# Optimization experiments

Hardware: AMD Instinct MI355X
Metric: run time of the kernel (lower is better)

## Reference

```python
import jax, jax.numpy as jnp
import numpy as np

B, S, D = 4, 1024, 512
H, DK, DV = 8, 64, 64
MAX_POS = 8  # relative position clamp; w_rpr maps d_k -> max_pos+1
EPS = 1e-6
TEMP = DK ** 0.5


def setup_inputs() -> dict:
    key = jax.random.key(0)
    ks = jax.random.split(key, 10)
    inp = {
        "q": jax.random.normal(ks[0], (B, S, D), jnp.float32),
        "k": jax.random.normal(ks[1], (B, S, D), jnp.float32),
        "v": jax.random.normal(ks[2], (B, S, D), jnp.float32),
        "dist": jax.random.randint(ks[3], (B, S, S), 0, 9, jnp.int32),
        # parameters (stored [in, out]; torch Linear applies x @ W.T)
        "Wq": jax.random.normal(ks[4], (D, H * DK), jnp.float32) / np.sqrt(D),
        "Wk": jax.random.normal(ks[5], (D, H * DK), jnp.float32) / np.sqrt(D),
        "Wv": jax.random.normal(ks[6], (D, H * DV), jnp.float32) / np.sqrt(D),
        "Wrpr": jax.random.normal(ks[7], (DK, MAX_POS + 1), jnp.float32) / np.sqrt(DK),
        "Wo": jax.random.normal(ks[8], (H * DV, D), jnp.float32) / np.sqrt(H * DV),
        "ln_g": jnp.ones((D,), jnp.float32),
        "ln_b": jnp.zeros((D,), jnp.float32),
    }
    return inp


def reference(q, k, v, dist, Wq, Wk, Wv, Wrpr, Wo, ln_g, ln_b):
    residual = q
    # LayerNorm on queries only (as in the original forward)
    mu = jnp.mean(q, axis=-1, keepdims=True)
    var = jnp.var(q, axis=-1, keepdims=True)
    qn = (q - mu) / jnp.sqrt(var + EPS) * ln_g + ln_b

    # projections -> [B, H, S, d]
    qh = (qn @ Wq).reshape(B, S, H, DK).transpose(0, 2, 1, 3) / TEMP
    kh = (k @ Wk).reshape(B, S, H, DK).transpose(0, 2, 1, 3)
    vh = (v @ Wv).reshape(B, S, H, DV).transpose(0, 2, 1, 3)

    # content scores [B,H,S,S]
    attn_k = jnp.einsum("bhqd,bhkd->bhqk", qh, kh)

    # relative-position bias: project q onto rpr embeddings then gather per (query, key)
    q_dot_rpr = qh @ Wrpr  # [B,H,S,max_pos+1]
    pos = jnp.minimum(dist, MAX_POS)  # [B,S,S]
    idx = jnp.broadcast_to(pos[:, None], (B, H, S, S))
    attn_rpr = jnp.take_along_axis(q_dot_rpr, idx, axis=-1)  # [B,H,S,S]

    attn = jax.nn.softmax(attn_k + attn_rpr, axis=-1)
    out = jnp.einsum("bhqk,bhkd->bhqd", attn, vh)  # [B,H,S,DV]
    out = out.transpose(0, 2, 1, 3).reshape(B, S, H * DV)
    out = out @ Wo + residual
    return out, attn
```

## Files before the change

kernel.cpp:

```cpp
#include <hip/hip_runtime.h>

#define BB 4
#define SS 1024
#define DDIM 512
#define HH 8
#define NR 9
#define QB 16
#define EPSV 1e-6f

typedef __attribute__((ext_vector_type(8))) short bf16x8;
typedef __attribute__((ext_vector_type(4))) short short4v;
typedef __attribute__((ext_vector_type(4))) float f32x4;

struct HL { short h; short l; };

__device__ inline float bfv(short h) {
    union { unsigned u; float f; } b; b.u = ((unsigned)(unsigned short)h) << 16; return b.f;
}
__device__ inline HL split2(float x) {
    union { float f; unsigned u; } a; a.f = x;
    unsigned short hu = (unsigned short)(a.u >> 16);
    union { unsigned u; float f; } b; b.u = ((unsigned)hu) << 16;
    float r = x - b.f;
    union { float f; unsigned u; } c; c.f = r;
    HL o; o.h = (short)hu; o.l = (short)(c.u >> 16);
    return o;
}

__global__ __launch_bounds__(128) void ln_split(const float* __restrict__ q,
                                                const float* __restrict__ g,
                                                const float* __restrict__ b,
                                                short* __restrict__ yh,
                                                short* __restrict__ yl) {
    int row = blockIdx.x;
    const float* x = q + (size_t)row * DDIM;
    int t = threadIdx.x;
    float4 v = ((const float4*)x)[t];
    float s  = v.x + v.y + v.z + v.w;
    float ss = v.x*v.x + v.y*v.y + v.z*v.z + v.w*v.w;
    __shared__ float rs[128], rss[128];
    rs[t] = s; rss[t] = ss; __syncthreads();
    for (int o = 64; o > 0; o >>= 1) {
        if (t < o) { rs[t] += rs[t+o]; rss[t] += rss[t+o]; }
        __syncthreads();
    }
    float mu  = rs[0] * (1.0f/DDIM);
    float var = rss[0] * (1.0f/DDIM) - mu*mu;
    float inv = rsqrtf(var + EPSV);
    float4 gg = ((const float4*)g)[t];
    float4 bb = ((const float4*)b)[t];
    float o0 = (v.x-mu)*inv*gg.x + bb.x;
    float o1 = (v.y-mu)*inv*gg.y + bb.y;
    float o2 = (v.z-mu)*inv*gg.z + bb.z;
    float o3 = (v.w-mu)*inv*gg.w + bb.w;
    short4v h4, l4;
    HL t0 = split2(o0); h4[0] = t0.h; l4[0] = t0.l;
    HL t1 = split2(o1); h4[1] = t1.h; l4[1] = t1.l;
    HL t2 = split2(o2); h4[2] = t2.h; l4[2] = t2.l;
    HL t3 = split2(o3); h4[3] = t3.h; l4[3] = t3.l;
    *(short4v*)&yh[(size_t)row*DDIM + t*4] = h4;
    *(short4v*)&yl[(size_t)row*DDIM + t*4] = l4;
}

__global__ __launch_bounds__(256) void split_x(const float* __restrict__ x,
                                               short* __restrict__ xh,
                                               short* __restrict__ xl) {
    int i = blockIdx.x*256 + threadIdx.x;
    float4 v = ((const float4*)x)[i];
    short4v h4, l4;
    HL t0 = split2(v.x); h4[0] = t0.h; l4[0] = t0.l;
    HL t1 = split2(v.y); h4[1] = t1.h; l4[1] = t1.l;
    HL t2 = split2(v.z); h4[2] = t2.h; l4[2] = t2.l;
    HL t3 = split2(v.w); h4[3] = t3.h; l4[3] = t3.l;
    *(short4v*)&xh[(size_t)i*4] = h4;
    *(short4v*)&xl[(size_t)i*4] = l4;
}

__global__ __launch_bounds__(256) void transW(const float* __restrict__ W,
                                              short* __restrict__ wth,
                                              short* __restrict__ wtl) {
    __shared__ float T[64][65];
    int n0 = blockIdx.x*64, k0 = blockIdx.y*64;
    int t = threadIdx.x;
    int kr = t >> 4, nc = (t & 15)*4;
#pragma unroll
    for (int i = 0; i < 4; ++i) {
        float4 v = *(const float4*)&W[(size_t)(k0 + kr + i*16)*DDIM + n0 + nc];
        T[nc+0][kr+i*16] = v.x;
        T[nc+1][kr+i*16] = v.y;
        T[nc+2][kr+i*16] = v.z;
        T[nc+3][kr+i*16] = v.w;
    }
    __syncthreads();
    int nr = t >> 2, kq = (t & 3)*16;
    short h8[16], l8[16];
#pragma unroll
    for (int j = 0; j < 16; ++j) {
        HL tt = split2(T[nr][kq+j]); h8[j] = tt.h; l8[j] = tt.l;
    }
    size_t base = (size_t)(n0+nr)*DDIM + k0 + kq;
#pragma unroll
    for (int j = 0; j < 2; ++j) {
        bf16x8 hv, lv;
#pragma unroll
        for (int e = 0; e < 8; ++e) { hv[e] = h8[j*8+e]; lv[e] = l8[j*8+e]; }
        *(bf16x8*)&wth[base + j*8] = hv;
        *(bf16x8*)&wtl[base + j*8] = lv;
    }
}

__global__ __launch_bounds__(256) void mm_gemm_qkv(
        const short* __restrict__ qnh, const short* __restrict__ qnl,
        const short* __restrict__ kxh, const short* __restrict__ kxl,
        const short* __restrict__ vxh, const short* __restrict__ vxl,
        const short* __restrict__ WqTh, const short* __restrict__ WqTl,
        const short* __restrict__ WkTh, const short* __restrict__ WkTl,
        const short* __restrict__ WvTh, const short* __restrict__ WvTl,
        short* __restrict__ qh_hi, short* __restrict__ qh_lo,
        short* __restrict__ kh_hi, short* __restrict__ kh_lo,
        short* __restrict__ vT_hi, short* __restrict__ vT_lo) {
    int z = blockIdx.z;
    const short *Ahi, *Alo, *Bhi, *Blo;
    short *o_hi, *o_lo;
    float scale = 1.0f;
    if (z == 0) { Ahi=qnh; Alo=qnl; Bhi=WqTh; Blo=WqTl; o_hi=qh_hi; o_lo=qh_lo; scale=0.125f; }
    else if (z == 1) { Ahi=kxh; Alo=kxl; Bhi=WkTh; Blo=WkTl; o_hi=kh_hi; o_lo=kh_lo; }
    else { Ahi=vxh; Alo=vxl; Bhi=WvTh; Blo=WvTl; o_hi=vT_hi; o_lo=vT_lo; }

    int n0 = blockIdx.x * 64, m0 = blockIdx.y * 64;
    int tid = threadIdx.x;
    int lane = tid & 63, w = tid >> 6;
    int wr = w >> 1, wc = w & 1;
    int r = lane & 15, ko = (lane >> 4) * 8;
    f32x4 acc[2][2] = {};
    int arow0 = m0 + wr*32 + r;
    int brow0 = n0 + wc*32 + r;
    for (int k0 = 0; k0 < 512; k0 += 32) {
        bf16x8 ah[2], al[2], bh[2], bl[2];
#pragma unroll
        for (int i = 0; i < 2; ++i) {
            size_t aoff = (size_t)(arow0 + i*16)*512 + k0 + ko;
            ah[i] = *(const bf16x8*)&Ahi[aoff];
            al[i] = *(const bf16x8*)&Alo[aoff];
            size_t boff = (size_t)(brow0 + i*16)*512 + k0 + ko;
            bh[i] = *(const bf16x8*)&Bhi[boff];
            bl[i] = *(const bf16x8*)&Blo[boff];
        }
#pragma unroll
        for (int i = 0; i < 2; ++i)
#pragma unroll
            for (int j = 0; j < 2; ++j) {
                acc[i][j] = __builtin_amdgcn_mfma_f32_16x16x32_bf16(ah[i], bh[j], acc[i][j], 0, 0, 0);
                acc[i][j] = __builtin_amdgcn_mfma_f32_16x16x32_bf16(ah[i], bl[j], acc[i][j], 0, 0, 0);
                acc[i][j] = __builtin_amdgcn_mfma_f32_16x16x32_bf16(al[i], bh[j], acc[i][j], 0, 0, 0);
            }
    }
    int rb = (lane >> 4) * 4;
    int cf = lane & 15;
#pragma unroll
    for (int i = 0; i < 2; ++i)
#pragma unroll
        for (int j = 0; j < 2; ++j)
#pragma unroll
            for (int rr = 0; rr < 4; ++rr) {
                int m = m0 + wr*32 + i*16 + rb + rr;
                int n = n0 + wc*32 + j*16 + cf;
                float v = acc[i][j][rr] * scale;
                HL tt = split2(v);
                int b = m >> 10, s = m & 1023;
                int hh = n >> 6, d = n & 63;
                size_t off;
                if (z == 2) off = ((size_t)((b*HH + hh)*64 + d))*SS + s;
                else        off = ((size_t)((b*HH + hh)*SS + s))*64 + d;
                o_hi[off] = tt.h;
                o_lo[off] = tt.l;
            }
}

__global__ __launch_bounds__(256) void mm_gemm_o(const short* __restrict__ Ahi,
                                                 const short* __restrict__ Alo,
                                                 const short* __restrict__ Bhi,
                                                 const short* __restrict__ Blo,
                                                 const float* __restrict__ res,
                                                 float* __restrict__ o_f) {
    int n0 = blockIdx.x * 64, m0 = blockIdx.y * 64;
    int tid = threadIdx.x;
    int lane = tid & 63, w = tid >> 6;
    int wr = w >> 1, wc = w & 1;
    int r = lane & 15, ko = (lane >> 4) * 8;
    f32x4 acc[2][2] = {};
    int arow0 = m0 + wr*32 + r;
    int brow0 = n0 + wc*32 + r;
    for (int k0 = 0; k0 < 512; k0 += 32) {
        bf16x8 ah[2], al[2], bh[2], bl[2];
#pragma unroll
        for (int i = 0; i < 2; ++i) {
            size_t aoff = (size_t)(arow0 + i*16)*512 + k0 + ko;
            ah[i] = *(const bf16x8*)&Ahi[aoff];
            al[i] = *(const bf16x8*)&Alo[aoff];
            size_t boff = (size_t)(brow0 + i*16)*512 + k0 + ko;
            bh[i] = *(const bf16x8*)&Bhi[boff];
            bl[i] = *(const bf16x8*)&Blo[boff];
        }
#pragma unroll
        for (int i = 0; i < 2; ++i)
#pragma unroll
            for (int j = 0; j < 2; ++j) {
                acc[i][j] = __builtin_amdgcn_mfma_f32_16x16x32_bf16(ah[i], bh[j], acc[i][j], 0, 0, 0);
                acc[i][j] = __builtin_amdgcn_mfma_f32_16x16x32_bf16(ah[i], bl[j], acc[i][j], 0, 0, 0);
                acc[i][j] = __builtin_amdgcn_mfma_f32_16x16x32_bf16(al[i], bh[j], acc[i][j], 0, 0, 0);
            }
    }
    int rb = (lane >> 4) * 4;
    int cf = lane & 15;
#pragma unroll
    for (int i = 0; i < 2; ++i)
#pragma unroll
        for (int j = 0; j < 2; ++j)
#pragma unroll
            for (int rr = 0; rr < 4; ++rr) {
                int m = m0 + wr*32 + i*16 + rb + rr;
                int n = n0 + wc*32 + j*16 + cf;
                o_f[(size_t)m*512 + n] = acc[i][j][rr] + res[(size_t)m*512 + n];
            }
}

__global__ __launch_bounds__(256) void qdr_kernel(const short* __restrict__ qhi,
                                                  const short* __restrict__ qlo,
                                                  const float* __restrict__ Wrpr,
                                                  float* __restrict__ qdr) {
    __shared__ float w[64*NR];
    int t = threadIdx.x;
    for (int i = t; i < 64*NR; i += 256) w[i] = Wrpr[i];
    __syncthreads();
    int row = blockIdx.x*256 + t;
    const short* qh = qhi + (size_t)row*64;
    const short* ql = qlo + (size_t)row*64;
    float acc[NR] = {};
#pragma unroll
    for (int d4 = 0; d4 < 16; ++d4) {
        short4v h4 = *(const short4v*)&qh[d4*4];
        short4v l4 = *(const short4v*)&ql[d4*4];
#pragma unroll
        for (int j = 0; j < 4; ++j) {
            float x = bfv(h4[j]) + bfv(l4[j]);
            const float* wr2 = &w[(d4*4+j)*NR];
#pragma unroll
            for (int p = 0; p < NR; ++p) acc[p] += x * wr2[p];
        }
    }
#pragma unroll
    for (int p = 0; p < NR; ++p) qdr[(size_t)row*NR + p] = acc[p];
}

__global__ __launch_bounds__(512, 4) void fused_attn(
        const short* __restrict__ qhi, const short* __restrict__ qlo,
        const short* __restrict__ khi, const short* __restrict__ klo,
        const short* __restrict__ vThi, const short* __restrict__ vTlo,
        const float* __restrict__ qdr,
        const int* __restrict__ dist,
        float* __restrict__ attn,
        short* __restrict__ pv_hi, short* __restrict__ pv_lo) {
    __shared__ float S_T[SS][QB+1];
    __shared__ float qd[QB][NR];
    __shared__ float inv_s[QB];
    __shared__ float PC[QB][68];
    int bh = blockIdx.y, b = bh >> 3, h = bh & 7;
    int q0 = blockIdx.x * QB;
    int tid = threadIdx.x, lane = tid & 63, w = tid >> 6;
    int r = lane & 15, g = lane >> 4, ko = g*8;

    if (tid < QB*NR) qd[tid/NR][tid%NR] = qdr[((size_t)bh*SS + q0)*NR + tid];

    const short* Qh = qhi + (size_t)bh*SS*64;
    const short* Ql = qlo + (size_t)bh*SS*64;
    const short* Kh = khi + (size_t)bh*SS*64;
    const short* Kl = klo + (size_t)bh*SS*64;
    {
        f32x4 acc[8];
#pragma unroll
        for (int t2 = 0; t2 < 8; ++t2) acc[t2] = (f32x4){0.f,0.f,0.f,0.f};
#pragma unroll
        for (int ks = 0; ks < 64; ks += 32) {
            bf16x8 ah = *(const bf16x8*)&Qh[(size_t)(q0+r)*64 + ks + ko];
            bf16x8 al = *(const bf16x8*)&Ql[(size_t)(q0+r)*64 + ks + ko];
#pragma unroll
            for (int ct = 0; ct < 8; ++ct) {
                int kc = w*128 + ct*16 + r;
                bf16x8 bh2 = *(const bf16x8*)&Kh[(size_t)kc*64 + ks + ko];
                bf16x8 bl2 = *(const bf16x8*)&Kl[(size_t)kc*64 + ks + ko];
                acc[ct] = __builtin_amdgcn_mfma_f32_16x16x32_bf16(ah, bh2, acc[ct], 0, 0, 0);
                acc[ct] = __builtin_amdgcn_mfma_f32_16x16x32_bf16(ah, bl2, acc[ct], 0, 0, 0);
                acc[ct] = __builtin_amdgcn_mfma_f32_16x16x32_bf16(al, bh2, acc[ct], 0, 0, 0);
            }
        }
#pragma unroll
        for (int ct = 0; ct < 8; ++ct)
#pragma unroll
            for (int rr = 0; rr < 4; ++rr)
                S_T[w*128 + ct*16 + r][g*4 + rr] = acc[ct][rr];
    }
    __syncthreads();

    int row = tid >> 5, c32 = tid & 31;
    const int* drow = &dist[((size_t)b*SS + q0 + row)*SS];
    float m = -1e30f;
    f32x4 sv[8];
#pragma unroll
    for (int c = 0; c < 8; ++c) {
        int col = c32*4 + c*128;
        int4 d4 = *(const int4*)&drow[col];
        f32x4 s4;
        s4[0] = S_T[col+0][row] + qd[row][d4.x > 8 ? 8 : d4.x];
        s4[1] = S_T[col+1][row] + qd[row][d4.y > 8 ? 8 : d4.y];
        s4[2] = S_T[col+2][row] + qd[row][d4.z > 8 ? 8 : d4.z];
        s4[3] = S_T[col+3][row] + qd[row][d4.w > 8 ? 8 : d4.w];
        sv[c] = s4;
        m = fmaxf(m, fmaxf(fmaxf(s4[0], s4[1]), fmaxf(s4[2], s4[3])));
    }
#pragma unroll
    for (int o = 1; o < 32; o <<= 1) m = fmaxf(m, __shfl_xor(m, o));
    float sum = 0.f;
#pragma unroll
    for (int c = 0; c < 8; ++c) {
        int col = c32*4 + c*128;
        f32x4 p4 = sv[c];
        p4[0] = expf(p4[0]-m); p4[1] = expf(p4[1]-m);
        p4[2] = expf(p4[2]-m); p4[3] = expf(p4[3]-m);
        sum += p4[0] + p4[1] + p4[2] + p4[3];
        S_T[col+0][row] = p4[0];
        S_T[col+1][row] = p4[1];
        S_T[col+2][row] = p4[2];
        S_T[col+3][row] = p4[3];
        sv[c] = p4;
    }
#pragma unroll
    for (int o = 1; o < 32; o <<= 1) sum += __shfl_xor(sum, o);
    float inv = 1.0f / sum;
    if (c32 == 0) inv_s[row] = inv;
    __syncthreads();

    float* arow = attn + ((size_t)bh*SS + q0 + row)*SS;
#pragma unroll
    for (int c = 0; c < 8; ++c) {
        int col = c32*4 + c*128;
        f32x4 o4 = sv[c];
        o4[0] *= inv; o4[1] *= inv; o4[2] *= inv; o4[3] *= inv;
        *(f32x4*)&arow[col] = o4;
    }

    int wd = w & 3, wk = w >> 2;
    const short* Vh = vThi + (size_t)bh*64*SS + (size_t)(wd*16 + r)*SS;
    const short* Vl = vTlo + (size_t)bh*64*SS + (size_t)(wd*16 + r)*SS;
    f32x4 oacc = (f32x4){0.f,0.f,0.f,0.f};
    for (int kbi = 0; kbi < 16; ++kbi) {
        int k8 = wk*512 + kbi*32 + ko;
        bf16x8 ah, al;
#pragma unroll
        for (int e = 0; e < 8; ++e) {
            HL tt = split2(S_T[k8 + e][r]);
            ah[e] = tt.h; al[e] = tt.l;
        }
        bf16x8 vh = *(const bf16x8*)&Vh[k8];
        bf16x8 vl = *(const bf16x8*)&Vl[k8];
        oacc = __builtin_amdgcn_mfma_f32_16x16x32_bf16(ah, vh, oacc, 0, 0, 0);
        oacc = __builtin_amdgcn_mfma_f32_16x16x32_bf16(ah, vl, oacc, 0, 0, 0);
        oacc = __builtin_amdgcn_mfma_f32_16x16x32_bf16(al, vh, oacc, 0, 0, 0);
    }
    if (wk == 1) {
#pragma unroll
        for (int rr = 0; rr < 4; ++rr) PC[g*4 + rr][wd*16 + r] = oacc[rr];
    }
    __syncthreads();
    if (wk == 0) {
#pragma unroll
        for (int rr = 0; rr < 4; ++rr) {
            int orow = g*4 + rr;
            float val = (oacc[rr] + PC[orow][wd*16 + r]) * inv_s[orow];
            HL tt = split2(val);
            size_t off = ((size_t)(b*SS + q0 + orow))*512 + h*64 + wd*16 + r;
            pv_hi[off] = tt.h; pv_lo[off] = tt.l;
        }
    }
}

extern "C" void kernel_launch(void* const* d_in, const int* in_sizes, int n_in,
                              void* d_out, int out_size, void* d_ws, size_t ws_size,
                              hipStream_t stream) {
    const float* q    = (const float*)d_in[0];
    const float* k    = (const float*)d_in[1];
    const float* v    = (const float*)d_in[2];
    const int*   dist = (const int*)d_in[3];
    const float* Wq   = (const float*)d_in[4];
    const float* Wk   = (const float*)d_in[5];
    const float* Wv   = (const float*)d_in[6];
    const float* Wrpr = (const float*)d_in[7];
    const float* Wo   = (const float*)d_in[8];
    const float* ln_g = (const float*)d_in[9];
    const float* ln_b = (const float*)d_in[10];

    float* out  = (float*)d_out;
    float* attn = out + (size_t)BB*SS*DDIM;

    const size_t NB = (size_t)BB*SS*DDIM;
    short* p = (short*)d_ws;
    short* qn_hi = p;            p += NB;
    short* qn_lo = p;            p += NB;
    short* kx_hi = p;            p += NB;
    short* kx_lo = p;            p += NB;
    short* vx_hi = p;            p += NB;
    short* vx_lo = p;            p += NB;
    short* qh_hi = p;            p += NB;
    short* qh_lo = p;            p += NB;
    short* kh_hi = p;            p += NB;
    short* kh_lo = p;            p += NB;
    short* vT_hi = p;            p += NB;
    short* vT_lo = p;            p += NB;
    short* WqT_h = p;            p += 262144;
    short* WqT_l = p;            p += 262144;
    short* WkT_h = p;            p += 262144;
    short* WkT_l = p;            p += 262144;
    short* WvT_h = p;            p += 262144;
    short* WvT_l = p;            p += 262144;
    short* WoT_h = p;            p += 262144;
    short* WoT_l = p;            p += 262144;
    float* qdrp  = (float*)p;
    short* pv_hi = qn_hi;
    short* pv_lo = qn_lo;

    ln_split<<<BB*SS, 128, 0, stream>>>(q, ln_g, ln_b, qn_hi, qn_lo);

    split_x<<<2048, 256, 0, stream>>>(k, kx_hi, kx_lo);
    split_x<<<2048, 256, 0, stream>>>(v, vx_hi, vx_lo);

    transW<<<dim3(8,8), 256, 0, stream>>>(Wq, WqT_h, WqT_l);
    transW<<<dim3(8,8), 256, 0, stream>>>(Wk, WkT_h, WkT_l);
    transW<<<dim3(8,8), 256, 0, stream>>>(Wv, WvT_h, WvT_l);
    transW<<<dim3(8,8), 256, 0, stream>>>(Wo, WoT_h, WoT_l);

    mm_gemm_qkv<<<dim3(8, 64, 3), 256, 0, stream>>>(
        qn_hi, qn_lo, kx_hi, kx_lo, vx_hi, vx_lo,
        WqT_h, WqT_l, WkT_h, WkT_l, WvT_h, WvT_l,
        qh_hi, qh_lo, kh_hi, kh_lo, vT_hi, vT_lo);

    qdr_kernel<<<128, 256, 0, stream>>>(qh_hi, qh_lo, Wrpr, qdrp);

    fused_attn<<<dim3(SS/QB, BB*HH), 512, 0, stream>>>(qh_hi, qh_lo, kh_hi, kh_lo,
                                                       vT_hi, vT_lo, qdrp, dist,
                                                       attn, pv_hi, pv_lo);

    mm_gemm_o<<<dim3(8, 64), 256, 0, stream>>>(pv_hi, pv_lo, WoT_h, WoT_l, q, out);
}
```

Measured before the change: 454.0 us.

## Stage GEMM tiles in LDS with register prefetch; store P as split bf16

The QKV and output-projection GEMMs now stage 64x64 hi/lo tiles of A and B in padded shared memory. Each thread prefetches the next K-slab into registers while the current slab is consumed, replacing per-wave strided global loads that re-read the same data. In the attention kernel, softmax probabilities are split into bf16 hi/lo once and written row-major to shared memory, reusing the score buffer. The P·V loop then issues vector LDS loads instead of eight strided scalar reads plus a split per element, at the cost of an extra barrier and more LDS traffic in the softmax write phase.

```diff
diff --git a/kernel.cpp b/kernel.cpp
--- a/kernel.cpp
+++ b/kernel.cpp
@@ -119,6 +119,7 @@
         short* __restrict__ qh_hi, short* __restrict__ qh_lo,
         short* __restrict__ kh_hi, short* __restrict__ kh_lo,
         short* __restrict__ vT_hi, short* __restrict__ vT_lo) {
+    __shared__ short As_h[64][72], As_l[64][72], Bs_h[64][72], Bs_l[64][72];
     int z = blockIdx.z;
     const short *Ahi, *Alo, *Bhi, *Blo;
     short *o_hi, *o_lo;
@@ -132,28 +133,46 @@
     int lane = tid & 63, w = tid >> 6;
     int wr = w >> 1, wc = w & 1;
     int r = lane & 15, ko = (lane >> 4) * 8;
+    int lrow = tid >> 2, lcol = (tid & 3) * 16;
+    const short* Ah0 = &Ahi[(size_t)(m0+lrow)*512 + lcol];
+    const short* Al0 = &Alo[(size_t)(m0+lrow)*512 + lcol];
+    const short* Bh0 = &Bhi[(size_t)(n0+lrow)*512 + lcol];
+    const short* Bl0 = &Blo[(size_t)(n0+lrow)*512 + lcol];
+    bf16x8 rah[2], ral[2], rbh[2], rbl[2];
+#define LOADREG(K) do { \
+        rah[0]=*(const bf16x8*)&Ah0[K]; rah[1]=*(const bf16x8*)&Ah0[(K)+8]; \
+        ral[0]=*(const bf16x8*)&Al0[K]; ral[1]=*(const bf16x8*)&Al0[(K)+8]; \
+        rbh[0]=*(const bf16x8*)&Bh0[K]; rbh[1]=*(const bf16x8*)&Bh0[(K)+8]; \
+        rbl[0]=*(const bf16x8*)&Bl0[K]; rbl[1]=*(const bf16x8*)&Bl0[(K)+8]; } while(0)
+    LOADREG(0);
     f32x4 acc[2][2] = {};
-    int arow0 = m0 + wr*32 + r;
-    int brow0 = n0 + wc*32 + r;
-    for (int k0 = 0; k0 < 512; k0 += 32) {
-        bf16x8 ah[2], al[2], bh[2], bl[2];
-#pragma unroll
-        for (int i = 0; i < 2; ++i) {
-            size_t aoff = (size_t)(arow0 + i*16)*512 + k0 + ko;
-            ah[i] = *(const bf16x8*)&Ahi[aoff];
-            al[i] = *(const bf16x8*)&Alo[aoff];
-            size_t boff = (size_t)(brow0 + i*16)*512 + k0 + ko;
-            bh[i] = *(const bf16x8*)&Bhi[boff];
-            bl[i] = *(const bf16x8*)&Blo[boff];
+    for (int k0 = 0; k0 < 512; k0 += 64) {
+        __syncthreads();
+        *(bf16x8*)&As_h[lrow][lcol] = rah[0]; *(bf16x8*)&As_h[lrow][lcol+8] = rah[1];
+        *(bf16x8*)&As_l[lrow][lcol] = ral[0]; *(bf16x8*)&As_l[lrow][lcol+8] = ral[1];
+        *(bf16x8*)&Bs_h[lrow][lcol] = rbh[0]; *(bf16x8*)&Bs_h[lrow][lcol+8] = rbh[1];
+        *(bf16x8*)&Bs_l[lrow][lcol] = rbl[0]; *(bf16x8*)&Bs_l[lrow][lcol+8] = rbl[1];
+        __syncthreads();
+        if (k0 < 448) LOADREG(k0 + 64);
+#pragma unroll
+        for (int ks = 0; ks < 64; ks += 32) {
+            bf16x8 ah[2], al[2], bh2[2], bl2[2];
+#pragma unroll
+            for (int i = 0; i < 2; ++i) {
+                ah[i]  = *(const bf16x8*)&As_h[wr*32 + i*16 + r][ks + ko];
+                al[i]  = *(const bf16x8*)&As_l[wr*32 + i*16 + r][ks + ko];
+                bh2[i] = *(const bf16x8*)&Bs_h[wc*32 + i*16 + r][ks + ko];
+                bl2[i] = *(const bf16x8*)&Bs_l[wc*32 + i*16 + r][ks + ko];
+            }
+#pragma unroll
+            for (int i = 0; i < 2; ++i)
+#pragma unroll
+                for (int j = 0; j < 2; ++j) {
+                    acc[i][j] = __builtin_amdgcn_mfma_f32_16x16x32_bf16(ah[i], bh2[j], acc[i][j], 0, 0, 0);
+                    acc[i][j] = __builtin_amdgcn_mfma_f32_16x16x32_bf16(ah[i], bl2[j], acc[i][j], 0, 0, 0);
+                    acc[i][j] = __builtin_amdgcn_mfma_f32_16x16x32_bf16(al[i], bh2[j], acc[i][j], 0, 0, 0);
+                }
         }
-#pragma unroll
-        for (int i = 0; i < 2; ++i)
-#pragma unroll
-            for (int j = 0; j < 2; ++j) {
-                acc[i][j] = __builtin_amdgcn_mfma_f32_16x16x32_bf16(ah[i], bh[j], acc[i][j], 0, 0, 0);
-                acc[i][j] = __builtin_amdgcn_mfma_f32_16x16x32_bf16(ah[i], bl[j], acc[i][j], 0, 0, 0);
-                acc[i][j] = __builtin_amdgcn_mfma_f32_16x16x32_bf16(al[i], bh[j], acc[i][j], 0, 0, 0);
-            }
     }
     int rb = (lane >> 4) * 4;
     int cf = lane & 15;
@@ -183,33 +202,47 @@
                                                  const short* __restrict__ Blo,
                                                  const float* __restrict__ res,
                                                  float* __restrict__ o_f) {
+    __shared__ short As_h[64][72], As_l[64][72], Bs_h[64][72], Bs_l[64][72];
     int n0 = blockIdx.x * 64, m0 = blockIdx.y * 64;
     int tid = threadIdx.x;
     int lane = tid & 63, w = tid >> 6;
     int wr = w >> 1, wc = w & 1;
     int r = lane & 15, ko = (lane >> 4) * 8;
+    int lrow = tid >> 2, lcol = (tid & 3) * 16;
+    const short* Ah0 = &Ahi[(size_t)(m0+lrow)*512 + lcol];
+    const short* Al0 = &Alo[(size_t)(m0+lrow)*512 + lcol];
+    const short* Bh0 = &Bhi[(size_t)(n0+lrow)*512 + lcol];
+    const short* Bl0 = &Blo[(size_t)(n0+lrow)*512 + lcol];
+    bf16x8 rah[2], ral[2], rbh[2], rbl[2];
+    LOADREG(0);
     f32x4 acc[2][2] = {};
-    int arow0 = m0 + wr*32 + r;
-    int brow0 = n0 + wc*32 + r;
-    for (int k0 = 0; k0 < 512; k0 += 32) {
-        bf16x8 ah[2], al[2], bh[2], bl[2];
-#pragma unroll
-        for (int i = 0; i < 2; ++i) {
-            size_t aoff = (size_t)(arow0 + i*16)*512 + k0 + ko;
-            ah[i] = *(const bf16x8*)&Ahi[aoff];
-            al[i] = *(const bf16x8*)&Alo[aoff];
-            size_t boff = (size_t)(brow0 + i*16)*512 + k0 + ko;
-            bh[i] = *(const bf16x8*)&Bhi[boff];
-            bl[i] = *(const bf16x8*)&Blo[boff];
+    for (int k0 = 0; k0 < 512; k0 += 64) {
+        __syncthreads();
+        *(bf16x8*)&As_h[lrow][lcol] = rah[0]; *(bf16x8*)&As_h[lrow][lcol+8] = rah[1];
+        *(bf16x8*)&As_l[lrow][lcol] = ral[0]; *(bf16x8*)&As_l[lrow][lcol+8] = ral[1];
+        *(bf16x8*)&Bs_h[lrow][lcol] = rbh[0]; *(bf16x8*)&Bs_h[lrow][lcol+8] = rbh[1];
+        *(bf16x8*)&Bs_l[lrow][lcol] = rbl[0]; *(bf16x8*)&Bs_l[lrow][lcol+8] = rbl[1];
+        __syncthreads();
+        if (k0 < 448) LOADREG(k0 + 64);
+#pragma unroll
+        for (int ks = 0; ks < 64; ks += 32) {
+            bf16x8 ah[2], al[2], bh2[2], bl2[2];
+#pragma unroll
+            for (int i = 0; i < 2; ++i) {
+                ah[i]  = *(const bf16x8*)&As_h[wr*32 + i*16 + r][ks + ko];
+                al[i]  = *(const bf16x8*)&As_l[wr*32 + i*16 + r][ks + ko];
+                bh2[i] = *(const bf16x8*)&Bs_h[wc*32 + i*16 + r][ks + ko];
+                bl2[i] = *(const bf16x8*)&Bs_l[wc*32 + i*16 + r][ks + ko];
+            }
+#pragma unroll
+            for (int i = 0; i < 2; ++i)
+#pragma unroll
+                for (int j = 0; j < 2; ++j) {
+                    acc[i][j] = __builtin_amdgcn_mfma_f32_16x16x32_bf16(ah[i], bh2[j], acc[i][j], 0, 0, 0);
+                    acc[i][j] = __builtin_amdgcn_mfma_f32_16x16x32_bf16(ah[i], bl2[j], acc[i][j], 0, 0, 0);
+                    acc[i][j] = __builtin_amdgcn_mfma_f32_16x16x32_bf16(al[i], bh2[j], acc[i][j], 0, 0, 0);
+                }
         }
-#pragma unroll
-        for (int i = 0; i < 2; ++i)
-#pragma unroll
-            for (int j = 0; j < 2; ++j) {
-                acc[i][j] = __builtin_amdgcn_mfma_f32_16x16x32_bf16(ah[i], bh[j], acc[i][j], 0, 0, 0);
-                acc[i][j] = __builtin_amdgcn_mfma_f32_16x16x32_bf16(ah[i], bl[j], acc[i][j], 0, 0, 0);
-                acc[i][j] = __builtin_amdgcn_mfma_f32_16x16x32_bf16(al[i], bh[j], acc[i][j], 0, 0, 0);
-            }
     }
     int rb = (lane >> 4) * 4;
     int cf = lane & 15;
@@ -261,10 +294,12 @@
         const int* __restrict__ dist,
         float* __restrict__ attn,
         short* __restrict__ pv_hi, short* __restrict__ pv_lo) {
-    __shared__ float S_T[SS][QB+1];
+    __shared__ float smem[SS*(QB+1)];
     __shared__ float qd[QB][NR];
     __shared__ float inv_s[QB];
     __shared__ float PC[QB][68];
+    short (*P_h)[1032] = (short(*)[1032])smem;
+    short (*P_l)[1032] = (short(*)[1032])((char*)smem + 16*1032*2);
     int bh = blockIdx.y, b = bh >> 3, h = bh & 7;
     int q0 = blockIdx.x * QB;
     int tid = threadIdx.x, lane = tid & 63, w = tid >> 6;
@@ -298,7 +333,7 @@
         for (int ct = 0; ct < 8; ++ct)
 #pragma unroll
             for (int rr = 0; rr < 4; ++rr)
-                S_T[w*128 + ct*16 + r][g*4 + rr] = acc[ct][rr];
+                smem[(w*128 + ct*16 + r)*17 + g*4 + rr] = acc[ct][rr];
     }
     __syncthreads();
 
@@ -311,13 +346,14 @@
         int col = c32*4 + c*128;
         int4 d4 = *(const int4*)&drow[col];
         f32x4 s4;
-        s4[0] = S_T[col+0][row] + qd[row][d4.x > 8 ? 8 : d4.x];
-        s4[1] = S_T[col+1][row] + qd[row][d4.y > 8 ? 8 : d4.y];
-        s4[2] = S_T[col+2][row] + qd[row][d4.z > 8 ? 8 : d4.z];
-        s4[3] = S_T[col+3][row] + qd[row][d4.w > 8 ? 8 : d4.w];
+        s4[0] = smem[(col+0)*17 + row] + qd[row][d4.x > 8 ? 8 : d4.x];
+        s4[1] = smem[(col+1)*17 + row] + qd[row][d4.y > 8 ? 8 : d4.y];
+        s4[2] = smem[(col+2)*17 + row] + qd[row][d4.z > 8 ? 8 : d4.z];
+        s4[3] = smem[(col+3)*17 + row] + qd[row][d4.w > 8 ? 8 : d4.w];
         sv[c] = s4;
         m = fmaxf(m, fmaxf(fmaxf(s4[0], s4[1]), fmaxf(s4[2], s4[3])));
     }
+    __syncthreads();
 #pragma unroll
     for (int o = 1; o < 32; o <<= 1) m = fmaxf(m, __shfl_xor(m, o));
     float sum = 0.f;
@@ -328,17 +364,19 @@
         p4[0] = expf(p4[0]-m); p4[1] = expf(p4[1]-m);
         p4[2] = expf(p4[2]-m); p4[3] = expf(p4[3]-m);
         sum += p4[0] + p4[1] + p4[2] + p4[3];
-        S_T[col+0][row] = p4[0];
-        S_T[col+1][row] = p4[1];
-        S_T[col+2][row] = p4[2];
-        S_T[col+3][row] = p4[3];
+        short4v ph, pl;
+        HL t0 = split2(p4[0]); ph[0] = t0.h; pl[0] = t0.l;
+        HL t1 = split2(p4[1]); ph[1] = t1.h; pl[1] = t1.l;
+        HL t2 = split2(p4[2]); ph[2] = t2.h; pl[2] = t2.l;
+        HL t3 = split2(p4[3]); ph[3] = t3.h; pl[3] = t3.l;
+        *(short4v*)&P_h[row][col] = ph;
+        *(short4v*)&P_l[row][col] = pl;
         sv[c] = p4;
     }
 #pragma unroll
     for (int o = 1; o < 32; o <<= 1) sum += __shfl_xor(sum, o);
     float inv = 1.0f / sum;
     if (c32 == 0) inv_s[row] = inv;
-    __syncthreads();
 
     float* arow = attn + ((size_t)bh*SS + q0 + row)*SS;
 #pragma unroll
@@ -348,6 +386,7 @@
         o4[0] *= inv; o4[1] *= inv; o4[2] *= inv; o4[3] *= inv;
         *(f32x4*)&arow[col] = o4;
     }
+    __syncthreads();
 
     int wd = w & 3, wk = w >> 2;
     const short* Vh = vThi + (size_t)bh*64*SS + (size_t)(wd*16 + r)*SS;
@@ -355,12 +394,8 @@
     f32x4 oacc = (f32x4){0.f,0.f,0.f,0.f};
     for (int kbi = 0; kbi < 16; ++kbi) {
         int k8 = wk*512 + kbi*32 + ko;
-        bf16x8 ah, al;
-#pragma unroll
-        for (int e = 0; e < 8; ++e) {
-            HL tt = split2(S_T[k8 + e][r]);
-            ah[e] = tt.h; al[e] = tt.l;
-        }
+        bf16x8 ah = *(const bf16x8*)&P_h[r][k8];
+        bf16x8 al = *(const bf16x8*)&P_l[r][k8];
         bf16x8 vh = *(const bf16x8*)&Vh[k8];
         bf16x8 vl = *(const bf16x8*)&Vl[k8];
         oacc = __builtin_amdgcn_mfma_f32_16x16x32_bf16(ah, vh, oacc, 0, 0, 0);
```

After: 384.9 us. -15.2%, faster.
